# Optimization experiments

Measured on AMD Instinct MI355X. Metric: run time of the kernel, lower is better.

The kernel has to match this reference:

```python
import jax, jax.numpy as jnp
import numpy as np

EPS = 1e-12

def _l2norm(x):
    # F.normalize(p=2, dim=-1) with torch's eps clamp
    n = jnp.sqrt(jnp.sum(x * x, axis=-1, keepdims=True))
    return x / jnp.maximum(n, EPS)

def setup_inputs() -> dict:
    key = jax.random.key(0)
    k1, k2, k3, k4 = jax.random.split(key, 4)
    B, Lq, Ld, H, D = 64, 32, 256, 768, 128
    Q_hidden = jax.random.normal(k1, (B, Lq, H), dtype=jnp.float32)
    D_hidden = jax.random.normal(k2, (B, Ld, H), dtype=jnp.float32)
    W = jax.random.normal(k3, (D, H), dtype=jnp.float32) * (1.0 / np.sqrt(H))
    d_mask = jax.random.randint(k4, (B, Ld), 0, 2).astype(bool)
    d_mask = d_mask.at[:, 0].set(True)  # every doc has >=1 valid token
    return {"Q_hidden": Q_hidden, "D_hidden": D_hidden, "W": W, "d_mask": d_mask}

def reference(Q_hidden, D_hidden, W, d_mask):
    # linear projection (no bias) + L2 normalize, as in query()/doc()
    Q = _l2norm(jnp.einsum('blh,dh->bld', Q_hidden, W))       # [B,Lq,D]
    Dv = _l2norm(jnp.einsum('blh,dh->bld', D_hidden, W))      # [B,Ld,D]
    Dv = Dv * d_mask[..., None].astype(Dv.dtype)              # zero padded/skiplist tokens
    # intra-batch cosine MaxSim: sim[b,c,q,n] = Q[b,q] . D[c,n]
    sim = jnp.einsum('bqd,cnd->bcqn', Q, Dv)                  # [B,B,Lq,Ld]
    sim = jnp.where(d_mask[None, :, None, :], sim, -jnp.inf)  # mask doc tokens
    return jnp.sum(jnp.max(sim, axis=-1), axis=-1)            # [B,B]
```

## Files before the change

kernel.cpp:

```cpp
#include <hip/hip_runtime.h>
#include <hip/hip_bf16.h>
#include <math.h>

typedef __attribute__((ext_vector_type(4))) float f32x4;
typedef __attribute__((ext_vector_type(8))) short bf16x8;

#define NB    64
#define LQ    32
#define LDOC  256
#define HDIM  768
#define DDIM  128
#define NTOK_Q (NB * LQ)
#define NTOK_D (NB * LDOC)
#define NTOK   (NTOK_Q + NTOK_D)

#define WS_OFF_W    0
#define WS_OFF_MASK 196608
#define WS_OFF_QN   212992
#define WS_OFF_DN   737280

__device__ inline short f2bf(float f) {
    unsigned u = __float_as_uint(f);
    u = (u + 0x7fffu + ((u >> 16) & 1u)) >> 16;
    return (short)u;
}

__global__ void prep(const float* __restrict__ W, short* __restrict__ Wbf,
                     const unsigned char* __restrict__ mraw,
                     unsigned short* __restrict__ maskT) {
    if (blockIdx.x < 96) {
        int i = blockIdx.x * 256 + threadIdx.x;
        float4 v = *(const float4*)(W + (size_t)i * 4);
        short4 o;
        o.x = f2bf(v.x); o.y = f2bf(v.y); o.z = f2bf(v.z); o.w = f2bf(v.w);
        *(short4*)(Wbf + (size_t)i * 4) = o;
        return;
    }
    __shared__ int dword_ok_s;
    if (threadIdx.x == 0) dword_ok_s = 1;
    __syncthreads();
    const unsigned* dw = (const unsigned*)mraw;
    int ok = 1;
    for (int i = threadIdx.x; i < 4096; i += 256) {
        unsigned v = dw[i];
        if (!(v == 0u || v == 1u || v == 0x3F800000u)) ok = 0;
    }
    if (!ok) atomicAnd(&dword_ok_s, 0);
    __syncthreads();
    const int isdw = dword_ok_s;
    for (int w = threadIdx.x; w < 1024; w += 256) {
        const int c = w >> 4, lcc = w & 15;
        unsigned bits = 0;
        if (isdw) {
            for (int nt = 0; nt < 16; ++nt)
                bits |= (dw[c * 256 + nt * 16 + lcc] ? 1u : 0u) << nt;
        } else {
            for (int nt = 0; nt < 16; ++nt)
                bits |= (mraw[c * 256 + nt * 16 + lcc] ? 1u : 0u) << nt;
        }
        maskT[w] = (unsigned short)bits;
    }
}

__global__ __launch_bounds__(256)
void proj_norm(const float* __restrict__ Qh, const float* __restrict__ Dh,
               const short* __restrict__ Wbf,
               short* __restrict__ Qn, short* __restrict__ Dn) {
    const int tid  = threadIdx.x;
    const int lane = tid & 63;
    const int wave = tid >> 6;
    const int g    = lane >> 4;
    const int lc   = lane & 15;
    const int wr   = wave >> 1;
    const int wc   = wave & 1;
    const int row0 = blockIdx.x * 32;

    const float* Asrc = (row0 < NTOK_Q) ? Qh + (size_t)row0 * HDIM
                                        : Dh + (size_t)(row0 - NTOK_Q) * HDIM;

    __shared__ alignas(16) float As[2][2048];
    __shared__ alignas(16) short Bs[2][8192];
    __shared__ float norms[2][2][16];

    auto STAGE = [&](int buf, int t) {
#pragma unroll
        for (int i = 0; i < 2; ++i) {
            const int sb = i * 256 + wave * 64;
            const int s  = sb + lane;
            const int row = s >> 4;
            const int cu  = (s & 15) ^ (row & 15);
            const float* ga = Asrc + (size_t)row * HDIM + t * 64 + cu * 4;
            __builtin_amdgcn_global_load_lds(
                (const __attribute__((address_space(1))) unsigned*)ga,
                (__attribute__((address_space(3))) unsigned*)((char*)&As[buf][0] + (size_t)sb * 16),
                16, 0, 0);
        }
#pragma unroll
        for (int i = 0; i < 4; ++i) {
            const int sb = i * 256 + wave * 64;
            const int s  = sb + lane;
            const int n  = s >> 3;
            const int c8 = (s & 7) ^ (n & 7);
            const short* gb = Wbf + (size_t)n * HDIM + t * 64 + c8 * 8;
            __builtin_amdgcn_global_load_lds(
                (const __attribute__((address_space(1))) unsigned*)gb,
                (__attribute__((address_space(3))) unsigned*)((char*)&Bs[buf][0] + (size_t)sb * 16),
                16, 0, 0);
        }
    };

    f32x4 acc[4];
#pragma unroll
    for (int nt = 0; nt < 4; ++nt) acc[nt] = (f32x4){0.f, 0.f, 0.f, 0.f};

    STAGE(0, 0);
    __syncthreads();

    for (int t = 0; t < 12; ++t) {
        const int cur = t & 1;
        if (t < 11) STAGE(cur ^ 1, t + 1);

        const float* Ab = &As[cur][0];
        const short* Bb = &Bs[cur][0];
#pragma unroll
        for (int ks = 0; ks < 2; ++ks) {
            bf16x8 bfr[4];
#pragma unroll
            for (int nt = 0; nt < 4; ++nt) {
                const int nl = wc * 64 + nt * 16 + lc;
                const int c8 = (ks * 4 + g) ^ (nl & 7);
                bfr[nt] = *(const bf16x8*)(Bb + (size_t)nl * 64 + c8 * 8);
            }
            const int rl = wr * 16 + lc;
            const int u0 = (ks * 8 + g * 2) ^ lc;
            const int u1 = (ks * 8 + g * 2 + 1) ^ lc;
            const float4 a0 = *(const float4*)(Ab + (size_t)rl * 64 + u0 * 4);
            const float4 a1 = *(const float4*)(Ab + (size_t)rl * 64 + u1 * 4);
            bf16x8 af;
            af[0] = f2bf(a0.x); af[1] = f2bf(a0.y); af[2] = f2bf(a0.z); af[3] = f2bf(a0.w);
            af[4] = f2bf(a1.x); af[5] = f2bf(a1.y); af[6] = f2bf(a1.z); af[7] = f2bf(a1.w);
#pragma unroll
            for (int nt = 0; nt < 4; ++nt)
                acc[nt] = __builtin_amdgcn_mfma_f32_16x16x32_bf16(af, bfr[nt], acc[nt], 0, 0, 0);
        }
        __syncthreads();
    }

    float part[4];
#pragma unroll
    for (int i = 0; i < 4; ++i) {
        float s = 0.f;
#pragma unroll
        for (int nt = 0; nt < 4; ++nt) s += acc[nt][i] * acc[nt][i];
        s += __shfl_xor(s, 1);
        s += __shfl_xor(s, 2);
        s += __shfl_xor(s, 4);
        s += __shfl_xor(s, 8);
        part[i] = s;
    }
    if (lc == 0) {
#pragma unroll
        for (int i = 0; i < 4; ++i) norms[wr][wc][g * 4 + i] = part[i];
    }
    __syncthreads();

    short* Obase = (row0 < NTOK_Q) ? Qn + (size_t)row0 * DDIM
                                   : Dn + (size_t)(row0 - NTOK_Q) * DDIM;
#pragma unroll
    for (int i = 0; i < 4; ++i) {
        const int rloc = g * 4 + i;
        const float tot = norms[wr][0][rloc] + norms[wr][1][rloc];
        const float inv = 1.f / fmaxf(sqrtf(tot), 1e-12f);
        short* dst = Obase + (size_t)(wr * 16 + rloc) * DDIM + wc * 64;
#pragma unroll
        for (int nt = 0; nt < 4; ++nt)
            dst[nt * 16 + lc] = f2bf(acc[nt][i] * inv);
    }
}

__global__ __launch_bounds__(512)
void maxsim(const short* __restrict__ Qn, const short* __restrict__ Dn,
            const unsigned short* __restrict__ maskT, float* __restrict__ out) {
    const int x  = blockIdx.x & 7;
    const int m8 = (blockIdx.x >> 3) & 7;
    const int bg = blockIdx.x >> 6;
    const int c  = x * 8 + m8;

    const int wave = threadIdx.x >> 6;
    const int lane = threadIdx.x & 63;
    const int g = lane >> 4, lc = lane & 15;

    __shared__ alignas(16) short Ds[2][4096 * 2];

    const short* dsrc = Dn + (size_t)c * LDOC * DDIM;

    auto STAGE = [&](int buf, int ch) {
#pragma unroll
        for (int i = 0; i < 2; ++i) {
            const int sb = wave * 128 + i * 64;
            const int s  = sb + lane;
            const int rowl = s >> 4;
            const int c16  = (s & 15) ^ (rowl & 15);
            const short* ga = dsrc + (size_t)(ch * 64 + rowl) * DDIM + c16 * 8;
            __builtin_amdgcn_global_load_lds(
                (const __attribute__((address_space(1))) unsigned*)ga,
                (__attribute__((address_space(3))) unsigned*)((char*)&Ds[buf][0] + (size_t)sb * 16),
                16, 0, 0);
        }
    };

    STAGE(0, 0);

    bf16x8 qf[2][4];
    const int qrow0 = bg * 256 + wave * 32;
#pragma unroll
    for (int m = 0; m < 2; ++m) {
        const short* qb = Qn + (size_t)(qrow0 + m * 16 + lc) * DDIM;
#pragma unroll
        for (int ks = 0; ks < 4; ++ks)
            qf[m][ks] = *(const bf16x8*)(qb + ks * 32 + g * 8);
    }
    const unsigned mbits = maskT[c * 16 + lc];

    __syncthreads();

    float rmax[2][4];
#pragma unroll
    for (int m = 0; m < 2; ++m)
#pragma unroll
        for (int i = 0; i < 4; ++i) rmax[m][i] = -INFINITY;

    for (int ch = 0; ch < 4; ++ch) {
        const int buf = ch & 1;
        if (ch < 3) STAGE(buf ^ 1, ch + 1);
        const short* Db = &Ds[buf][0];
#pragma unroll
        for (int j = 0; j < 4; ++j) {
            const int rowl = j * 16 + lc;
            bf16x8 bf[4];
#pragma unroll
            for (int ks = 0; ks < 4; ++ks) {
                const int c16 = (ks * 4 + g) ^ lc;
                bf[ks] = *(const bf16x8*)(Db + (size_t)rowl * DDIM + c16 * 8);
            }
            const bool on = (mbits >> (ch * 4 + j)) & 1;
#pragma unroll
            for (int m = 0; m < 2; ++m) {
                f32x4 acc = (f32x4){0.f, 0.f, 0.f, 0.f};
#pragma unroll
                for (int ks = 0; ks < 4; ++ks)
                    acc = __builtin_amdgcn_mfma_f32_16x16x32_bf16(qf[m][ks], bf[ks], acc, 0, 0, 0);
#pragma unroll
                for (int i = 0; i < 4; ++i)
                    rmax[m][i] = on ? fmaxf(rmax[m][i], acc[i]) : rmax[m][i];
            }
        }
        __syncthreads();
    }

    float s = 0.f;
#pragma unroll
    for (int m = 0; m < 2; ++m)
#pragma unroll
        for (int i = 0; i < 4; ++i) {
            float r = rmax[m][i];
            r = fmaxf(r, __shfl_xor(r, 1));
            r = fmaxf(r, __shfl_xor(r, 2));
            r = fmaxf(r, __shfl_xor(r, 4));
            r = fmaxf(r, __shfl_xor(r, 8));
            s += r;
        }
    s += __shfl_xor(s, 16);
    s += __shfl_xor(s, 32);

    if (lane == 0) {
        const int b = bg * 8 + wave;
        out[(size_t)b * NB + c] = s;
    }
}

extern "C" void kernel_launch(void* const* d_in, const int* in_sizes, int n_in,
                              void* d_out, int out_size, void* d_ws, size_t ws_size,
                              hipStream_t stream) {
    const float* Qh = (const float*)d_in[0];
    const float* Dh = (const float*)d_in[1];
    const float* W  = (const float*)d_in[2];
    const unsigned char* dm = (const unsigned char*)d_in[3];
    float* out = (float*)d_out;
    char* ws = (char*)d_ws;

    short*          Wbf   = (short*)(ws + WS_OFF_W);
    unsigned short* maskT = (unsigned short*)(ws + WS_OFF_MASK);
    short*          Qn    = (short*)(ws + WS_OFF_QN);
    short*          Dn    = (short*)(ws + WS_OFF_DN);

    prep<<<97, 256, 0, stream>>>(W, Wbf, dm, maskT);
    proj_norm<<<NTOK / 32, 256, 0, stream>>>(Qh, Dh, Wbf, Qn, Dn);
    maxsim<<<512, 512, 0, stream>>>(Qn, Dn, maskT, out);
}
```

Before: 42.63 us.

## Fuse W bf16 conversion and mask packing into projection kernel, drop prep launch

Removes the separate prep kernel. Each projection block now loads fp32 W through registers, converts it to bf16 and writes it swizzled into LDS, with the load issued before the MFMAs and the LDS write after them. Block 0 also packs the doc mask at its end. This saves one kernel launch and the Wbf round trip through memory. In exchange, every block reads twice as many W bytes, spends VALU time on conversion, and holds more registers.

```diff
diff --git a/kernel.cpp b/kernel.cpp
--- a/kernel.cpp
+++ b/kernel.cpp
@@ -14,7 +14,6 @@
 #define NTOK_D (NB * LDOC)
 #define NTOK   (NTOK_Q + NTOK_D)
 
-#define WS_OFF_W    0
 #define WS_OFF_MASK 196608
 #define WS_OFF_QN   212992
 #define WS_OFF_DN   737280
@@ -25,47 +24,12 @@
     return (short)u;
 }
 
-__global__ void prep(const float* __restrict__ W, short* __restrict__ Wbf,
-                     const unsigned char* __restrict__ mraw,
-                     unsigned short* __restrict__ maskT) {
-    if (blockIdx.x < 96) {
-        int i = blockIdx.x * 256 + threadIdx.x;
-        float4 v = *(const float4*)(W + (size_t)i * 4);
-        short4 o;
-        o.x = f2bf(v.x); o.y = f2bf(v.y); o.z = f2bf(v.z); o.w = f2bf(v.w);
-        *(short4*)(Wbf + (size_t)i * 4) = o;
-        return;
-    }
-    __shared__ int dword_ok_s;
-    if (threadIdx.x == 0) dword_ok_s = 1;
-    __syncthreads();
-    const unsigned* dw = (const unsigned*)mraw;
-    int ok = 1;
-    for (int i = threadIdx.x; i < 4096; i += 256) {
-        unsigned v = dw[i];
-        if (!(v == 0u || v == 1u || v == 0x3F800000u)) ok = 0;
-    }
-    if (!ok) atomicAnd(&dword_ok_s, 0);
-    __syncthreads();
-    const int isdw = dword_ok_s;
-    for (int w = threadIdx.x; w < 1024; w += 256) {
-        const int c = w >> 4, lcc = w & 15;
-        unsigned bits = 0;
-        if (isdw) {
-            for (int nt = 0; nt < 16; ++nt)
-                bits |= (dw[c * 256 + nt * 16 + lcc] ? 1u : 0u) << nt;
-        } else {
-            for (int nt = 0; nt < 16; ++nt)
-                bits |= (mraw[c * 256 + nt * 16 + lcc] ? 1u : 0u) << nt;
-        }
-        maskT[w] = (unsigned short)bits;
-    }
-}
-
 __global__ __launch_bounds__(256)
 void proj_norm(const float* __restrict__ Qh, const float* __restrict__ Dh,
-               const short* __restrict__ Wbf,
-               short* __restrict__ Qn, short* __restrict__ Dn) {
+               const float* __restrict__ W,
+               short* __restrict__ Qn, short* __restrict__ Dn,
+               const unsigned char* __restrict__ mraw,
+               unsigned short* __restrict__ maskT) {
     const int tid  = threadIdx.x;
     const int lane = tid & 63;
     const int wave = tid >> 6;
@@ -82,7 +46,7 @@
     __shared__ alignas(16) short Bs[2][8192];
     __shared__ float norms[2][2][16];
 
-    auto STAGE = [&](int buf, int t) {
+    auto STAGE_A = [&](int buf, int t) {
 #pragma unroll
         for (int i = 0; i < 2; ++i) {
             const int sb = i * 256 + wave * 64;
@@ -95,30 +59,49 @@
                 (__attribute__((address_space(3))) unsigned*)((char*)&As[buf][0] + (size_t)sb * 16),
                 16, 0, 0);
         }
+    };
+
+    float4 bl[4][2];
+    auto BLOAD = [&](int t) {
 #pragma unroll
         for (int i = 0; i < 4; ++i) {
-            const int sb = i * 256 + wave * 64;
-            const int s  = sb + lane;
-            const int n  = s >> 3;
-            const int c8 = (s & 7) ^ (n & 7);
-            const short* gb = Wbf + (size_t)n * HDIM + t * 64 + c8 * 8;
-            __builtin_amdgcn_global_load_lds(
-                (const __attribute__((address_space(1))) unsigned*)gb,
-                (__attribute__((address_space(3))) unsigned*)((char*)&Bs[buf][0] + (size_t)sb * 16),
-                16, 0, 0);
+            const int s = i * 256 + tid;
+            const int n = s >> 3, u = s & 7;
+            const float* gw = W + (size_t)n * HDIM + t * 64 + u * 8;
+            bl[i][0] = *(const float4*)(gw);
+            bl[i][1] = *(const float4*)(gw + 4);
         }
     };
+    auto BWRITE = [&](int buf) {
+#pragma unroll
+        for (int i = 0; i < 4; ++i) {
+            const int s = i * 256 + tid;
+            const int n = s >> 3, u = s & 7;
+            bf16x8 v;
+            v[0] = f2bf(bl[i][0].x); v[1] = f2bf(bl[i][0].y);
+            v[2] = f2bf(bl[i][0].z); v[3] = f2bf(bl[i][0].w);
+            v[4] = f2bf(bl[i][1].x); v[5] = f2bf(bl[i][1].y);
+            v[6] = f2bf(bl[i][1].z); v[7] = f2bf(bl[i][1].w);
+            *(bf16x8*)(&Bs[buf][(size_t)n * 64 + (size_t)(u ^ (n & 7)) * 8]) = v;
+        }
+    };
 
     f32x4 acc[4];
 #pragma unroll
     for (int nt = 0; nt < 4; ++nt) acc[nt] = (f32x4){0.f, 0.f, 0.f, 0.f};
 
-    STAGE(0, 0);
+    STAGE_A(0, 0);
+    BLOAD(0);
+    BWRITE(0);
     __syncthreads();
 
     for (int t = 0; t < 12; ++t) {
         const int cur = t & 1;
-        if (t < 11) STAGE(cur ^ 1, t + 1);
+        if (t < 11) {
+            STAGE_A(cur ^ 1, t + 1);
+            BLOAD(t + 1);
+        }
+        __builtin_amdgcn_sched_barrier(0);
 
         const float* Ab = &As[cur][0];
         const short* Bb = &Bs[cur][0];
@@ -143,6 +126,7 @@
             for (int nt = 0; nt < 4; ++nt)
                 acc[nt] = __builtin_amdgcn_mfma_f32_16x16x32_bf16(af, bfr[nt], acc[nt], 0, 0, 0);
         }
+        if (t < 11) BWRITE(cur ^ 1);
         __syncthreads();
     }
 
@@ -175,6 +159,33 @@
 #pragma unroll
         for (int nt = 0; nt < 4; ++nt)
             dst[nt * 16 + lc] = f2bf(acc[nt][i] * inv);
+    }
+
+    if (blockIdx.x == 0) {
+        __shared__ int dword_ok_s;
+        if (tid == 0) dword_ok_s = 1;
+        __syncthreads();
+        const unsigned* dw = (const unsigned*)mraw;
+        int ok = 1;
+        for (int i = tid; i < 4096; i += 256) {
+            unsigned v = dw[i];
+            if (!(v == 0u || v == 1u || v == 0x3F800000u)) ok = 0;
+        }
+        if (!ok) atomicAnd(&dword_ok_s, 0);
+        __syncthreads();
+        const int isdw = dword_ok_s;
+        for (int w = tid; w < 1024; w += 256) {
+            const int c = w >> 4, lcc = w & 15;
+            unsigned bits = 0;
+            if (isdw) {
+                for (int nt = 0; nt < 16; ++nt)
+                    bits |= (dw[c * 256 + nt * 16 + lcc] ? 1u : 0u) << nt;
+            } else {
+                for (int nt = 0; nt < 16; ++nt)
+                    bits |= (mraw[c * 256 + nt * 16 + lcc] ? 1u : 0u) << nt;
+            }
+            maskT[w] = (unsigned short)bits;
+        }
     }
 }
 
@@ -289,12 +300,10 @@
     float* out = (float*)d_out;
     char* ws = (char*)d_ws;
 
-    short*          Wbf   = (short*)(ws + WS_OFF_W);
     unsigned short* maskT = (unsigned short*)(ws + WS_OFF_MASK);
     short*          Qn    = (short*)(ws + WS_OFF_QN);
     short*          Dn    = (short*)(ws + WS_OFF_DN);
 
-    prep<<<97, 256, 0, stream>>>(W, Wbf, dm, maskT);
-    proj_norm<<<NTOK / 32, 256, 0, stream>>>(Qh, Dh, Wbf, Qn, Dn);
+    proj_norm<<<NTOK / 32, 256, 0, stream>>>(Qh, Dh, W, Qn, Dn, dm, maskT);
     maxsim<<<512, 512, 0, stream>>>(Qn, Dn, maskT, out);
 }
```

New measurement: 44.28 us. +3.9%, slower.

## Triple-buffer projection GEMM with 512 threads and fine-grained vmcnt waits

Applied to the files above, without the earlier changes.

Raises the projection kernel's block size from 256 to 512 threads, splitting the 128 output columns across four waves per row group instead of two. It switches from double to triple buffering, prefetching two K-tiles ahead. Explicit s_waitcnt vmcnt counts with raw s_barrier replace the full __syncthreads, so loads stay in flight across iterations. This adds LDS use and per-wave halves the MFMA work, which may lower occupancy or raise the relative sync cost.

```diff
diff --git a/kernel.cpp b/kernel.cpp
--- a/kernel.cpp
+++ b/kernel.cpp
@@ -62,7 +62,7 @@
     }
 }
 
-__global__ __launch_bounds__(256)
+__global__ __launch_bounds__(512)
 void proj_norm(const float* __restrict__ Qh, const float* __restrict__ Dh,
                const short* __restrict__ Wbf,
                short* __restrict__ Qn, short* __restrict__ Dn) {
@@ -71,63 +71,65 @@
     const int wave = tid >> 6;
     const int g    = lane >> 4;
     const int lc   = lane & 15;
-    const int wr   = wave >> 1;
-    const int wc   = wave & 1;
+    const int wr   = wave >> 2;
+    const int wq   = wave & 3;
     const int row0 = blockIdx.x * 32;
 
     const float* Asrc = (row0 < NTOK_Q) ? Qh + (size_t)row0 * HDIM
                                         : Dh + (size_t)(row0 - NTOK_Q) * HDIM;
 
-    __shared__ alignas(16) float As[2][2048];
-    __shared__ alignas(16) short Bs[2][8192];
-    __shared__ float norms[2][2][16];
+    __shared__ alignas(16) float As[3][2048];
+    __shared__ alignas(16) short Bs[3][8192];
+    __shared__ float norms[2][4][16];
 
     auto STAGE = [&](int buf, int t) {
-#pragma unroll
-        for (int i = 0; i < 2; ++i) {
-            const int sb = i * 256 + wave * 64;
-            const int s  = sb + lane;
+        {
+            const int s   = tid;
             const int row = s >> 4;
             const int cu  = (s & 15) ^ (row & 15);
             const float* ga = Asrc + (size_t)row * HDIM + t * 64 + cu * 4;
             __builtin_amdgcn_global_load_lds(
                 (const __attribute__((address_space(1))) unsigned*)ga,
-                (__attribute__((address_space(3))) unsigned*)((char*)&As[buf][0] + (size_t)sb * 16),
+                (__attribute__((address_space(3))) unsigned*)((char*)&As[buf][0] + (size_t)(wave * 64) * 16),
                 16, 0, 0);
         }
 #pragma unroll
-        for (int i = 0; i < 4; ++i) {
-            const int sb = i * 256 + wave * 64;
-            const int s  = sb + lane;
+        for (int i = 0; i < 2; ++i) {
+            const int s  = i * 512 + tid;
             const int n  = s >> 3;
             const int c8 = (s & 7) ^ (n & 7);
             const short* gb = Wbf + (size_t)n * HDIM + t * 64 + c8 * 8;
             __builtin_amdgcn_global_load_lds(
                 (const __attribute__((address_space(1))) unsigned*)gb,
-                (__attribute__((address_space(3))) unsigned*)((char*)&Bs[buf][0] + (size_t)sb * 16),
+                (__attribute__((address_space(3))) unsigned*)((char*)&Bs[buf][0] + (size_t)(i * 512 + wave * 64) * 16),
                 16, 0, 0);
         }
     };
 
-    f32x4 acc[4];
-#pragma unroll
-    for (int nt = 0; nt < 4; ++nt) acc[nt] = (f32x4){0.f, 0.f, 0.f, 0.f};
+    f32x4 acc[2];
+    acc[0] = (f32x4){0.f, 0.f, 0.f, 0.f};
+    acc[1] = (f32x4){0.f, 0.f, 0.f, 0.f};
 
     STAGE(0, 0);
-    __syncthreads();
-
+    STAGE(1, 1);
+    asm volatile("s_waitcnt vmcnt(3)" ::: "memory");
+    __builtin_amdgcn_sched_barrier(0);
+    __builtin_amdgcn_s_barrier();
+    __builtin_amdgcn_sched_barrier(0);
+
+#pragma unroll
     for (int t = 0; t < 12; ++t) {
-        const int cur = t & 1;
-        if (t < 11) STAGE(cur ^ 1, t + 1);
-
-        const float* Ab = &As[cur][0];
-        const short* Bb = &Bs[cur][0];
+        if (t + 2 < 12) STAGE((t + 2) % 3, t + 2);
+        __builtin_amdgcn_sched_barrier(0);
+
+        const float* Ab = &As[t % 3][0];
+        const short* Bb = &Bs[t % 3][0];
 #pragma unroll
         for (int ks = 0; ks < 2; ++ks) {
-            bf16x8 bfr[4];
-#pragma unroll
-            for (int nt = 0; nt < 4; ++nt) {
-                const int nl = wc * 64 + nt * 16 + lc;
+            bf16x8 bfr[2];
+#pragma unroll
+            for (int nt = 0; nt < 2; ++nt) {
+                const int nl = wq * 32 + nt * 16 + lc;
                 const int c8 = (ks * 4 + g) ^ (nl & 7);
                 bfr[nt] = *(const bf16x8*)(Bb + (size_t)nl * 64 + c8 * 8);
             }
@@ -140,18 +142,27 @@
             af[0] = f2bf(a0.x); af[1] = f2bf(a0.y); af[2] = f2bf(a0.z); af[3] = f2bf(a0.w);
             af[4] = f2bf(a1.x); af[5] = f2bf(a1.y); af[6] = f2bf(a1.z); af[7] = f2bf(a1.w);
 #pragma unroll
-            for (int nt = 0; nt < 4; ++nt)
+            for (int nt = 0; nt < 2; ++nt)
                 acc[nt] = __builtin_amdgcn_mfma_f32_16x16x32_bf16(af, bfr[nt], acc[nt], 0, 0, 0);
         }
-        __syncthreads();
-    }
+
+        if (t <= 9) {
+            asm volatile("s_waitcnt vmcnt(3)" ::: "memory");
+        } else if (t == 10) {
+            asm volatile("s_waitcnt vmcnt(0)" ::: "memory");
+        }
+        __builtin_amdgcn_sched_barrier(0);
+        if (t < 11) {
+            __builtin_amdgcn_s_barrier();
+            __builtin_amdgcn_sched_barrier(0);
+        }
+    }
+    __syncthreads();
 
     float part[4];
 #pragma unroll
     for (int i = 0; i < 4; ++i) {
-        float s = 0.f;
-#pragma unroll
-        for (int nt = 0; nt < 4; ++nt) s += acc[nt][i] * acc[nt][i];
+        float s = acc[0][i] * acc[0][i] + acc[1][i] * acc[1][i];
         s += __shfl_xor(s, 1);
         s += __shfl_xor(s, 2);
         s += __shfl_xor(s, 4);
@@ -160,7 +171,7 @@
     }
     if (lc == 0) {
 #pragma unroll
-        for (int i = 0; i < 4; ++i) norms[wr][wc][g * 4 + i] = part[i];
+        for (int i = 0; i < 4; ++i) norms[wr][wq][g * 4 + i] = part[i];
     }
     __syncthreads();
 
@@ -169,11 +180,12 @@
 #pragma unroll
     for (int i = 0; i < 4; ++i) {
         const int rloc = g * 4 + i;
-        const float tot = norms[wr][0][rloc] + norms[wr][1][rloc];
+        const float tot = norms[wr][0][rloc] + norms[wr][1][rloc]
+                        + norms[wr][2][rloc] + norms[wr][3][rloc];
         const float inv = 1.f / fmaxf(sqrtf(tot), 1e-12f);
-        short* dst = Obase + (size_t)(wr * 16 + rloc) * DDIM + wc * 64;
-#pragma unroll
-        for (int nt = 0; nt < 4; ++nt)
+        short* dst = Obase + (size_t)(wr * 16 + rloc) * DDIM + wq * 32;
+#pragma unroll
+        for (int nt = 0; nt < 2; ++nt)
             dst[nt * 16 + lc] = f2bf(acc[nt][i] * inv);
     }
 }
@@ -295,6 +307,6 @@
     short*          Dn    = (short*)(ws + WS_OFF_DN);
 
     prep<<<97, 256, 0, stream>>>(W, Wbf, dm, maskT);
-    proj_norm<<<NTOK / 32, 256, 0, stream>>>(Qh, Dh, Wbf, Qn, Dn);
+    proj_norm<<<NTOK / 32, 512, 0, stream>>>(Qh, Dh, Wbf, Qn, Dn);
     maxsim<<<512, 512, 0, stream>>>(Qn, Dn, maskT, out);
 }
```

Result: slower. 49.45 us (+16.0%).

## Stage tiles through registers instead of direct global-to-LDS loads; store A as bf16

Applied to the files above, without the earlier changes.

Both kernels stop using global_load_lds and instead prefetch the next tile into registers, then write it to LDS after the current tile's MFMAs, with a sched_barrier to keep the loads issued early. In proj_norm the fp32 activation tile is converted to bf16 once at store time. That halves the A tile's LDS footprint and removes the repeated per-wave conversion in the inner loop. The cost is more registers and explicit LDS write instructions, which could reduce overlap or occupancy.

```diff
diff --git a/kernel.cpp b/kernel.cpp
--- a/kernel.cpp
+++ b/kernel.cpp
@@ -78,49 +78,62 @@
     const float* Asrc = (row0 < NTOK_Q) ? Qh + (size_t)row0 * HDIM
                                         : Dh + (size_t)(row0 - NTOK_Q) * HDIM;
 
-    __shared__ alignas(16) float As[2][2048];
+    __shared__ alignas(16) short As[2][2048];
     __shared__ alignas(16) short Bs[2][8192];
     __shared__ float norms[2][2][16];
 
-    auto STAGE = [&](int buf, int t) {
-#pragma unroll
-        for (int i = 0; i < 2; ++i) {
-            const int sb = i * 256 + wave * 64;
-            const int s  = sb + lane;
-            const int row = s >> 4;
-            const int cu  = (s & 15) ^ (row & 15);
-            const float* ga = Asrc + (size_t)row * HDIM + t * 64 + cu * 4;
-            __builtin_amdgcn_global_load_lds(
-                (const __attribute__((address_space(1))) unsigned*)ga,
-                (__attribute__((address_space(3))) unsigned*)((char*)&As[buf][0] + (size_t)sb * 16),
-                16, 0, 0);
-        }
-#pragma unroll
-        for (int i = 0; i < 4; ++i) {
-            const int sb = i * 256 + wave * 64;
-            const int s  = sb + lane;
-            const int n  = s >> 3;
-            const int c8 = (s & 7) ^ (n & 7);
-            const short* gb = Wbf + (size_t)n * HDIM + t * 64 + c8 * 8;
-            __builtin_amdgcn_global_load_lds(
-                (const __attribute__((address_space(1))) unsigned*)gb,
-                (__attribute__((address_space(3))) unsigned*)((char*)&Bs[buf][0] + (size_t)sb * 16),
-                16, 0, 0);
-        }
+    const int arow = tid >> 3, au = tid & 7;
+    const float* aga  = Asrc + (size_t)arow * HDIM + au * 8;
+    const int    adst = arow * 64 + (au ^ (arow & 7)) * 8;
+    const int n0 = tid >> 3,           u0 = tid & 7;
+    const int n1 = (256 + tid) >> 3,   u1 = u0;
+    const int n2 = (512 + tid) >> 3,   u2 = u0;
+    const int n3 = (768 + tid) >> 3,   u3 = u0;
+    const short* bga0 = Wbf + (size_t)n0 * HDIM + u0 * 8;
+    const short* bga1 = Wbf + (size_t)n1 * HDIM + u1 * 8;
+    const short* bga2 = Wbf + (size_t)n2 * HDIM + u2 * 8;
+    const short* bga3 = Wbf + (size_t)n3 * HDIM + u3 * 8;
+    const int bd0 = n0 * 64 + (u0 ^ (n0 & 7)) * 8;
+    const int bd1 = n1 * 64 + (u1 ^ (n1 & 7)) * 8;
+    const int bd2 = n2 * 64 + (u2 ^ (n2 & 7)) * 8;
+    const int bd3 = n3 * 64 + (u3 ^ (n3 & 7)) * 8;
+
+    float4 ar0, ar1;
+    bf16x8 br0, br1, br2, br3;
+
+    auto LOADS = [&](int t) {
+        ar0 = *(const float4*)(aga + t * 64);
+        ar1 = *(const float4*)(aga + t * 64 + 4);
+        br0 = *(const bf16x8*)(bga0 + t * 64);
+        br1 = *(const bf16x8*)(bga1 + t * 64);
+        br2 = *(const bf16x8*)(bga2 + t * 64);
+        br3 = *(const bf16x8*)(bga3 + t * 64);
     };
+    auto WRITES = [&](int buf) {
+        bf16x8 av;
+        av[0] = f2bf(ar0.x); av[1] = f2bf(ar0.y); av[2] = f2bf(ar0.z); av[3] = f2bf(ar0.w);
+        av[4] = f2bf(ar1.x); av[5] = f2bf(ar1.y); av[6] = f2bf(ar1.z); av[7] = f2bf(ar1.w);
+        *(bf16x8*)(&As[buf][adst]) = av;
+        *(bf16x8*)(&Bs[buf][bd0]) = br0;
+        *(bf16x8*)(&Bs[buf][bd1]) = br1;
+        *(bf16x8*)(&Bs[buf][bd2]) = br2;
+        *(bf16x8*)(&Bs[buf][bd3]) = br3;
+    };
 
     f32x4 acc[4];
 #pragma unroll
     for (int nt = 0; nt < 4; ++nt) acc[nt] = (f32x4){0.f, 0.f, 0.f, 0.f};
 
-    STAGE(0, 0);
+    LOADS(0);
+    WRITES(0);
     __syncthreads();
 
     for (int t = 0; t < 12; ++t) {
         const int cur = t & 1;
-        if (t < 11) STAGE(cur ^ 1, t + 1);
-
-        const float* Ab = &As[cur][0];
+        if (t < 11) LOADS(t + 1);
+        __builtin_amdgcn_sched_barrier(0);
+
+        const short* Ab = &As[cur][0];
         const short* Bb = &Bs[cur][0];
 #pragma unroll
         for (int ks = 0; ks < 2; ++ks) {
@@ -132,17 +145,13 @@
                 bfr[nt] = *(const bf16x8*)(Bb + (size_t)nl * 64 + c8 * 8);
             }
             const int rl = wr * 16 + lc;
-            const int u0 = (ks * 8 + g * 2) ^ lc;
-            const int u1 = (ks * 8 + g * 2 + 1) ^ lc;
-            const float4 a0 = *(const float4*)(Ab + (size_t)rl * 64 + u0 * 4);
-            const float4 a1 = *(const float4*)(Ab + (size_t)rl * 64 + u1 * 4);
-            bf16x8 af;
-            af[0] = f2bf(a0.x); af[1] = f2bf(a0.y); af[2] = f2bf(a0.z); af[3] = f2bf(a0.w);
-            af[4] = f2bf(a1.x); af[5] = f2bf(a1.y); af[6] = f2bf(a1.z); af[7] = f2bf(a1.w);
+            const int ua = (ks * 4 + g) ^ (rl & 7);
+            bf16x8 af = *(const bf16x8*)(Ab + (size_t)rl * 64 + ua * 8);
 #pragma unroll
             for (int nt = 0; nt < 4; ++nt)
                 acc[nt] = __builtin_amdgcn_mfma_f32_16x16x32_bf16(af, bfr[nt], acc[nt], 0, 0, 0);
         }
+        if (t < 11) WRITES(cur ^ 1);
         __syncthreads();
     }
 
@@ -186,30 +195,32 @@
     const int bg = blockIdx.x >> 6;
     const int c  = x * 8 + m8;
 
-    const int wave = threadIdx.x >> 6;
-    const int lane = threadIdx.x & 63;
+    const int tid  = threadIdx.x;
+    const int wave = tid >> 6;
+    const int lane = tid & 63;
     const int g = lane >> 4, lc = lane & 15;
 
-    __shared__ alignas(16) short Ds[2][4096 * 2];
+    __shared__ alignas(16) short Ds[2][8192];
 
     const short* dsrc = Dn + (size_t)c * LDOC * DDIM;
 
-    auto STAGE = [&](int buf, int ch) {
-#pragma unroll
-        for (int i = 0; i < 2; ++i) {
-            const int sb = wave * 128 + i * 64;
-            const int s  = sb + lane;
-            const int rowl = s >> 4;
-            const int c16  = (s & 15) ^ (rowl & 15);
-            const short* ga = dsrc + (size_t)(ch * 64 + rowl) * DDIM + c16 * 8;
-            __builtin_amdgcn_global_load_lds(
-                (const __attribute__((address_space(1))) unsigned*)ga,
-                (__attribute__((address_space(3))) unsigned*)((char*)&Ds[buf][0] + (size_t)sb * 16),
-                16, 0, 0);
-        }
+    const int r0 = tid >> 4,          v0 = tid & 15;
+    const int r1 = (512 + tid) >> 4,  v1 = v0;
+    const int dd0 = r0 * DDIM + (v0 ^ (r0 & 15)) * 8;
+    const int dd1 = r1 * DDIM + (v1 ^ (r1 & 15)) * 8;
+    bf16x8 dr0, dr1;
+
+    auto LOADS = [&](int ch) {
+        dr0 = *(const bf16x8*)(dsrc + (size_t)(ch * 64 + r0) * DDIM + v0 * 8);
+        dr1 = *(const bf16x8*)(dsrc + (size_t)(ch * 64 + r1) * DDIM + v1 * 8);
     };
-
-    STAGE(0, 0);
+    auto WRITES = [&](int buf) {
+        *(bf16x8*)(&Ds[buf][dd0]) = dr0;
+        *(bf16x8*)(&Ds[buf][dd1]) = dr1;
+    };
+
+    LOADS(0);
+    WRITES(0);
 
     bf16x8 qf[2][4];
     const int qrow0 = bg * 256 + wave * 32;
@@ -232,7 +243,8 @@
 
     for (int ch = 0; ch < 4; ++ch) {
         const int buf = ch & 1;
-        if (ch < 3) STAGE(buf ^ 1, ch + 1);
+        if (ch < 3) LOADS(ch + 1);
+        __builtin_amdgcn_sched_barrier(0);
         const short* Db = &Ds[buf][0];
 #pragma unroll
         for (int j = 0; j < 4; ++j) {
@@ -255,6 +267,7 @@
                     rmax[m][i] = on ? fmaxf(rmax[m][i], acc[i]) : rmax[m][i];
             }
         }
+        if (ch < 3) WRITES(buf ^ 1);
         __syncthreads();
     }
 
```

Result: faster. 41.52 us (-2.6%).
